# Optimization experiments

Hardware: AMD Instinct MI355X
Metric: run time of the kernel (lower is better)

Reference implementation:

```python
import jax, jax.numpy as jnp
import numpy as np

B = 16          # graphs per batch
NN = 2000       # nodes per graph (num_nodes)
N = B * NN      # total nodes in the batched graph
F_IN = 128      # input node features
H, C = 4, 64    # heads, per-head out channels (both GAT layers)
HC = H * C
DEG = 12        # average degree per node
FC1, FC2, OUT = 512, 128, 1
FC_IN = 6 * NN  # len(which_layer) = 6


def setup_inputs() -> dict:
    key = jax.random.key(0)
    ks = jax.random.split(key, 32)

    def g(i, shape, s=0.05):
        return jax.random.normal(ks[i], shape, jnp.float32) * s

    # within-graph random edges, no self loops (GATConv removes then re-adds them)
    src_l = jax.random.randint(ks[0], (B, NN * DEG), 0, NN)
    off = jax.random.randint(ks[1], (B, NN * DEG), 1, NN)
    dst_l = (src_l + off) % NN
    goff = (jnp.arange(B) * NN)[:, None]
    edge_index = jnp.stack([(src_l + goff).reshape(-1),
                            (dst_l + goff).reshape(-1)]).astype(jnp.int32)

    return {
        "x": g(2, (N, F_IN), 1.0),
        "W1": g(3, (F_IN, HC)), "att_src1": g(4, (H, C)), "att_dst1": g(5, (H, C)),
        "b1": jnp.zeros((HC,), jnp.float32),
        "W2": g(6, (HC, HC)), "att_src2": g(7, (H, C)), "att_dst2": g(8, (H, C)),
        "b2": jnp.zeros((HC,), jnp.float32),
        "pw1": g(9, (HC, 1)), "pb1": jnp.zeros((1,), jnp.float32),
        "pw2": g(10, (HC, 1)), "pb2": jnp.zeros((1,), jnp.float32),
        "ln_w": jnp.ones((NN,), jnp.float32), "ln_b": jnp.zeros((NN,), jnp.float32),
        "sex_emb": g(11, (2, NN)), "mut_emb": g(12, (4, NN)),
        "age_w": g(13, (NN,)), "age_b": jnp.zeros((NN,), jnp.float32),
        "fw1": g(14, (FC_IN, FC1)), "fb1": jnp.zeros((FC1,), jnp.float32),
        "fw2": g(15, (FC1, FC2)), "fb2": jnp.zeros((FC2,), jnp.float32),
        "fw3": g(16, (FC2, OUT)), "fb3": jnp.zeros((OUT,), jnp.float32),
        "age": jax.random.uniform(ks[17], (B,), jnp.float32),
        "edge_index": edge_index,
        "sex": jax.random.randint(ks[18], (B,), 0, 2),
        "mutation": jax.random.randint(ks[19], (B,), 0, 4),
    }


def _layer_norm(x, w, b, eps=1e-5):
    mu = jnp.mean(x, -1, keepdims=True)
    var = jnp.mean((x - mu) ** 2, -1, keepdims=True)
    return (x - mu) / jnp.sqrt(var + eps) * w + b


def _gat_conv(x, W, att_src, att_dst, bias, src, dst):
    h = (x @ W).reshape(N, H, C)                         # [N,H,C]
    a_s = jnp.sum(h * att_src[None], -1)                 # [N,H]
    a_d = jnp.sum(h * att_dst[None], -1)                 # [N,H]
    alpha = jax.nn.leaky_relu(a_s[src] + a_d[dst], 0.2)  # [E,H]
    m = jax.ops.segment_max(alpha, dst, num_segments=N)  # segment softmax over dst
    e = jnp.exp(alpha - m[dst])
    denom = jax.ops.segment_sum(e, dst, num_segments=N)
    a = e / (denom[dst] + 1e-16)
    out = jax.ops.segment_sum(a[:, :, None] * h[src], dst, num_segments=N)
    return out.reshape(N, HC) + bias


def _forward(x, W1, att_src1, att_dst1, b1, W2, att_src2, att_dst2, b2,
             pw1, pb1, pw2, pb2, ln_w, ln_b, sex_emb, mut_emb, age_w, age_b,
             fw1, fb1, fw2, fb2, fw3, fb3, age, edge_index, sex, mutation):
    loop = jnp.arange(N, dtype=edge_index.dtype)         # self loops added by GATConv
    src = jnp.concatenate([edge_index[0], loop])
    dst = jnp.concatenate([edge_index[1], loop])

    x0 = jnp.mean(x, -1).reshape(B, NN)                  # to_dense_batch(mean(x,-1))

    h = jax.nn.relu(_gat_conv(x, W1, att_src1, att_dst1, b1, src, dst))
    x1 = (h @ pw1 + pb1).squeeze(-1).reshape(B, NN)
    h = jax.nn.relu(_gat_conv(h, W2, att_src2, att_dst2, b2, src, dst))
    x2 = (h @ pw2 + pb2).squeeze(-1).reshape(B, NN)

    x0 = _layer_norm(x0, ln_w, ln_b)
    x1 = _layer_norm(x1, ln_w, ln_b)
    x2 = _layer_norm(x2, ln_w, ln_b)
    ms = jnp.concatenate([x0, x1, x2], axis=1)           # [B, 3*NN]

    demo = jnp.concatenate([sex_emb[sex], mut_emb[mutation],
                            age[:, None] * age_w[None, :] + age_b], axis=1)
    t = jnp.concatenate([demo, ms], axis=1)              # [B, 6*NN]
    t = jax.nn.relu(t @ fw1 + fb1)
    t = jax.nn.relu(t @ fw2 + fb2)
    pred = t @ fw3 + fb3                                 # [B, 1]
    return pred, x0, x1, x2, ms


def reference(x, W1, att_src1, att_dst1, b1, W2, att_src2, att_dst2, b2,
              pw1, pb1, pw2, pb2, ln_w, ln_b, sex_emb, mut_emb, age_w, age_b,
              fw1, fb1, fw2, fb2, fw3, fb3, age, edge_index, sex, mutation):
    return _forward(x, W1, att_src1, att_dst1, b1, W2, att_src2, att_dst2, b2,
                    pw1, pb1, pw2, pb2, ln_w, ln_b, sex_emb, mut_emb, age_w, age_b,
                    fw1, fb1, fw2, fb2, fw3, fb3, age, edge_index, sex, mutation)
```

## Files before the change

kernel.cpp:

```cpp
#include <hip/hip_runtime.h>
#include <math.h>

#define NTOT   32000
#define NNODE  2000
#define NB     16
#define FIN    128
#define HCDIM  256
#define NH     4
#define FC1DIM 512
#define FC2DIM 128
#define FCIN   12000
#define NCH    250
#define KCC    48
#define CAP    64
#define BK     32
#define LPITCH 40
#define TRB2   24
#define DEMOB  375

typedef __attribute__((ext_vector_type(8))) short bf16x8;
typedef __attribute__((ext_vector_type(4))) float f32x4;

__device__ inline float4 ld4(const float* p){ return *reinterpret_cast<const float4*>(p); }
__device__ inline void st4(float* p, float4 v){ *reinterpret_cast<float4*>(p) = v; }
__device__ inline float4 add4(float4 a, float4 b){ return make_float4(a.x+b.x,a.y+b.y,a.z+b.z,a.w+b.w); }
__device__ inline float lrelu(float x){ return x > 0.f ? x : 0.2f*x; }
__device__ inline float4 leaky4(float4 a){ return make_float4(lrelu(a.x),lrelu(a.y),lrelu(a.z),lrelu(a.w)); }
__device__ inline float4 exp4u(float4 a){ return make_float4(__expf(a.x),__expf(a.y),__expf(a.z),__expf(a.w)); }
__device__ inline float dot4(float4 a, float4 b){ return a.x*b.x + a.y*b.y + a.z*b.z + a.w*b.w; }
__device__ inline float selh(float4 v, int h){ return h==0 ? v.x : (h==1 ? v.y : (h==2 ? v.z : v.w)); }

__device__ inline unsigned short f2bf(float f){
  unsigned int u = __float_as_uint(f);
  u += 0x7FFFu + ((u >> 16) & 1u);
  return (unsigned short)(u >> 16);
}
__device__ inline unsigned int pk2bf(float a, float b){
  return (unsigned int)f2bf(a) | ((unsigned int)f2bf(b) << 16);
}
__device__ inline float bf2f(unsigned short h){
  return __uint_as_float(((unsigned int)h) << 16);
}
__device__ inline float4 ldbf4(const unsigned short* p){
  ushort4 v = *reinterpret_cast<const ushort4*>(p);
  return make_float4(bf2f(v.x), bf2f(v.y), bf2f(v.z), bf2f(v.w));
}

__global__ __launch_bounds__(256) void k_zero(int* __restrict__ cnt){
  int i = blockIdx.x*256 + threadIdx.x;
  if(i < NTOT) cnt[i] = 0;
}

__device__ __forceinline__ void ln_impl(const float* __restrict__ src,
                                        const float* __restrict__ lnw,
                                        const float* __restrict__ lnb,
                                        float* __restrict__ o1,
                                        float* __restrict__ o2,
                                        float* __restrict__ o3,
                                        float* red){
  int tid = threadIdx.x, lane = tid & 63, wv = tid >> 6;
  float s = 0.f, ss = 0.f;
  for(int i = tid; i < NNODE; i += 256){ float v = src[i]; s += v; ss += v*v; }
  #pragma unroll
  for(int off=1; off<64; off<<=1){ s += __shfl_xor(s, off); ss += __shfl_xor(ss, off); }
  if(lane == 0){ red[wv] = s; red[4+wv] = ss; }
  __syncthreads();
  s  = red[0]+red[1]+red[2]+red[3];
  ss = red[4]+red[5]+red[6]+red[7];
  float mu  = s * (1.0f/NNODE);
  float var = ss * (1.0f/NNODE) - mu*mu;
  float inv = 1.0f / sqrtf(var + 1e-5f);
  for(int i = tid; i < NNODE; i += 256){
    float v = (src[i]-mu)*inv*lnw[i] + lnb[i];
    o1[i] = v; o2[i] = v; o3[i] = v;
  }
}

__global__ void k_misc(const int* __restrict__ src, const int* __restrict__ dst,
                       int* __restrict__ cnt, int* __restrict__ col, int e0, int eb,
                       const float* __restrict__ W1, const float* __restrict__ W2,
                       unsigned short* __restrict__ W1t, unsigned short* __restrict__ W2t,
                       const float* __restrict__ sexemb, const float* __restrict__ mutemb,
                       const float* __restrict__ agew, const float* __restrict__ ageb,
                       const float* __restrict__ age, const int* __restrict__ sex,
                       const int* __restrict__ mut, float* __restrict__ t){
  __shared__ float tile[64][65];
  int blk = blockIdx.x;
  if(blk < eb){
    int i = blk*256 + threadIdx.x;
    if(i < e0){
      int d = dst[i];
      int slot = atomicAdd(&cnt[d], 1);
      if(slot < CAP) col[(d<<6) + slot] = src[i];
    }
  } else if(blk < eb + TRB2){
    int tb = blk - eb;
    int wv = threadIdx.x >> 6, lane = threadIdx.x & 63;
    if(tb < 8){
      int tk = tb >> 2, tn = tb & 3;
      int k0 = tk*64, n0 = tn*64;
      #pragma unroll
      for(int q=0;q<16;q++){
        int row = q*4 + wv;
        tile[row][lane] = W1[(size_t)(k0+row)*HCDIM + n0 + lane];
      }
      __syncthreads();
      #pragma unroll
      for(int q=0;q<16;q++){
        int row = q*4 + wv;
        W1t[(size_t)(n0+row)*FIN + k0 + lane] = f2bf(tile[lane][row]);
      }
    } else {
      int t2 = tb - 8;
      int tk = t2 >> 2, tn = t2 & 3;
      int k0 = tk*64, n0 = tn*64;
      #pragma unroll
      for(int q=0;q<16;q++){
        int row = q*4 + wv;
        tile[row][lane] = W2[(size_t)(k0+row)*HCDIM + n0 + lane];
      }
      __syncthreads();
      #pragma unroll
      for(int q=0;q<16;q++){
        int row = q*4 + wv;
        W2t[(size_t)(n0+row)*HCDIM + k0 + lane] = f2bf(tile[lane][row]);
      }
    }
  } else {
    int i = (blk - eb - TRB2)*256 + threadIdx.x;
    int b = i / (3*NNODE);
    int j = i - b*(3*NNODE);
    float v;
    if(j < NNODE)          v = sexemb[sex[b]*NNODE + j];
    else if(j < 2*NNODE)   v = mutemb[mut[b]*NNODE + (j - NNODE)];
    else                   v = age[b]*agew[j - 2*NNODE] + ageb[j - 2*NNODE];
    t[b*FCIN + j] = v;
  }
}

template<int AF32>
__global__ __launch_bounds__(256) void k_gemm_bf(const void* __restrict__ Av,
                                                 const unsigned short* __restrict__ Bt,
                                                 unsigned short* __restrict__ C,
                                                 const float* __restrict__ attS,
                                                 const float* __restrict__ attD,
                                                 float* __restrict__ a_s,
                                                 float* __restrict__ a_d,
                                                 float* __restrict__ x0r,
                                                 int M, int K){
  const unsigned short* A = (const unsigned short*)Av;
  const float*         Af = (const float*)Av;
  __shared__ unsigned short As[128][LPITCH];
  __shared__ unsigned short Bs[128][LPITCH];
  int tid = threadIdx.x;
  int lane = tid & 63, wv = tid >> 6;
  int wm = (wv & 1)*64, wn = (wv >> 1)*64;
  int m0 = blockIdx.y*128, n0 = blockIdx.x*128;
  int l15 = lane & 15, lq = lane >> 4;
  f32x4 acc[4][4];
  #pragma unroll
  for(int i=0;i<4;i++)
    #pragma unroll
    for(int j=0;j<4;j++)
      acc[i][j] = (f32x4){0.f,0.f,0.f,0.f};

  int r = tid >> 2, c = (tid & 3)*8;
  float rs1 = 0.f, rs2 = 0.f;
  for(int k0 = 0; k0 < K; k0 += BK){
    if(AF32){
      const float* pa  = Af + (size_t)(m0+r)*K + k0 + c;
      const float* pa2 = Af + (size_t)(m0+r+64)*K + k0 + c;
      float4 u0 = ld4(pa),  u1 = ld4(pa+4);
      float4 v0 = ld4(pa2), v1 = ld4(pa2+4);
      rs1 += (u0.x+u0.y+u0.z+u0.w) + (u1.x+u1.y+u1.z+u1.w);
      rs2 += (v0.x+v0.y+v0.z+v0.w) + (v1.x+v1.y+v1.z+v1.w);
      uint4 w0, w1;
      w0.x = pk2bf(u0.x,u0.y); w0.y = pk2bf(u0.z,u0.w);
      w0.z = pk2bf(u1.x,u1.y); w0.w = pk2bf(u1.z,u1.w);
      w1.x = pk2bf(v0.x,v0.y); w1.y = pk2bf(v0.z,v0.w);
      w1.z = pk2bf(v1.x,v1.y); w1.w = pk2bf(v1.z,v1.w);
      *reinterpret_cast<uint4*>(&As[r][c])    = w0;
      *reinterpret_cast<uint4*>(&As[r+64][c]) = w1;
    } else {
      *reinterpret_cast<uint4*>(&As[r][c])    = *reinterpret_cast<const uint4*>(A  + (size_t)(m0+r)*K + k0 + c);
      *reinterpret_cast<uint4*>(&As[r+64][c]) = *reinterpret_cast<const uint4*>(A  + (size_t)(m0+r+64)*K + k0 + c);
    }
    *reinterpret_cast<uint4*>(&Bs[r][c])    = *reinterpret_cast<const uint4*>(Bt + (size_t)(n0+r)*K + k0 + c);
    *reinterpret_cast<uint4*>(&Bs[r+64][c]) = *reinterpret_cast<const uint4*>(Bt + (size_t)(n0+r+64)*K + k0 + c);
    __syncthreads();
    bf16x8 af[4], bfr[4];
    #pragma unroll
    for(int i=0;i<4;i++){
      af[i]  = *reinterpret_cast<const bf16x8*>(&As[wm + i*16 + l15][lq*8]);
      bfr[i] = *reinterpret_cast<const bf16x8*>(&Bs[wn + i*16 + l15][lq*8]);
    }
    #pragma unroll
    for(int mi=0;mi<4;mi++)
      #pragma unroll
      for(int ni=0;ni<4;ni++)
        acc[mi][ni] = __builtin_amdgcn_mfma_f32_16x16x32_bf16(af[mi], bfr[ni], acc[mi][ni], 0, 0, 0);
    __syncthreads();
  }
  if(AF32 && n0 == 0){
    float s1 = rs1, s2 = rs2;
    s1 += __shfl_xor(s1,1); s1 += __shfl_xor(s1,2);
    s2 += __shfl_xor(s2,1); s2 += __shfl_xor(s2,2);
    if((tid & 3) == 0){
      x0r[m0 + r]      = s1 * (1.0f/FIN);
      x0r[m0 + r + 64] = s2 * (1.0f/FIN);
    }
  }
  #pragma unroll
  for(int mi=0;mi<4;mi++){
    #pragma unroll
    for(int ni=0;ni<4;ni++){
      int cn = n0 + wn + ni*16 + l15;
      #pragma unroll
      for(int rg=0;rg<4;rg++){
        int rm = m0 + wm + mi*16 + lq*4 + rg;
        C[(size_t)rm*HCDIM + cn] = f2bf(acc[mi][ni][rg]);
      }
    }
  }
  int head = (n0 + wn) >> 6;
  float avs[4], avd[4];
  #pragma unroll
  for(int ni=0;ni<4;ni++){
    int cc = ni*16 + l15;
    avs[ni] = attS[head*64 + cc];
    avd[ni] = attD[head*64 + cc];
  }
  #pragma unroll
  for(int mi=0;mi<4;mi++){
    #pragma unroll
    for(int rg=0;rg<4;rg++){
      float ps = 0.f, pd = 0.f;
      #pragma unroll
      for(int ni=0;ni<4;ni++){
        float v = acc[mi][ni][rg];
        ps = fmaf(avs[ni], v, ps);
        pd = fmaf(avd[ni], v, pd);
      }
      #pragma unroll
      for(int off=1; off<16; off<<=1){
        ps += __shfl_xor(ps, off);
        pd += __shfl_xor(pd, off);
      }
      if(l15 == 0){
        int rm = m0 + wm + mi*16 + lq*4 + rg;
        a_s[rm*4 + head] = ps;
        a_d[rm*4 + head] = pd;
      }
    }
  }
}

template<int STORE>
__global__ __launch_bounds__(256) void k_agg(const unsigned short* __restrict__ hpre,
                                             const float* __restrict__ a_s,
                                             const float* __restrict__ a_d,
                                             const int* __restrict__ cnt,
                                             const int* __restrict__ col,
                                             const float* __restrict__ bias,
                                             const float* __restrict__ pw,
                                             const float* __restrict__ pb,
                                             unsigned short* __restrict__ hout,
                                             float* __restrict__ xraw,
                                             const float* __restrict__ lnsrc,
                                             const float* __restrict__ lnw,
                                             const float* __restrict__ lnb,
                                             float* __restrict__ out,
                                             float* __restrict__ t,
                                             int which){
  __shared__ float4 ew[4][CAP];
  __shared__ int    cols[4][CAP+1];
  __shared__ float  lred[8];
  int bx = blockIdx.x;
  if(bx < 16){
    int b = bx;
    ln_impl(lnsrc + b*NNODE, lnw, lnb,
            out + 16 + which*(NB*NNODE) + b*NNODE,
            out + 16 + 3*(NB*NNODE) + b*(3*NNODE) + which*NNODE,
            t + b*FCIN + 3*NNODE + which*NNODE, lred);
    return;
  }
  int tid = threadIdx.x;
  int lane = tid & 63, wv = tid >> 6;
  int blk  = bx - 16;
  int xcd  = blk & 7;
  int slot = blk >> 3;
  int half = slot / 500;
  int g    = xcd + 8*half;
  int n    = g*NNODE + (slot - half*500)*4 + wv;
  int f0 = lane*4;
  int hl = lane >> 4;
  float4 ad   = ld4(a_d + n*4);
  float4 asn  = ld4(a_s + n*4);
  float4 eself = exp4u(leaky4(add4(asn, ad)));
  int deg = min(cnt[n], CAP);
  int base = n << 6;
  if(lane < deg){
    int s = col[base + lane];
    cols[wv][lane] = s;
    ew[wv][lane] = exp4u(leaky4(add4(ld4(a_s + s*4), ad)));
  } else {
    cols[wv][lane] = n;
  }
  if(lane == 0) cols[wv][CAP] = n;
  float es = selh(eself, hl);
  float dsum = es;
  float4 hv = ldbf4(hpre + (size_t)n*HCDIM + f0);
  float4 acc = make_float4(es*hv.x, es*hv.y, es*hv.z, es*hv.w);
  const float* ewf = (const float*)&ew[wv][0];
  const int*   cwf = &cols[wv][0];
  float4 h2 = ldbf4(hpre + (size_t)cwf[0]*HCDIM + f0);
  for(int e = 0; e < deg; e++){
    int sn = cwf[e+1];
    float4 hn = ldbf4(hpre + (size_t)sn*HCDIM + f0);
    float w = ewf[e*4 + hl];
    dsum += w;
    acc.x = fmaf(w, h2.x, acc.x); acc.y = fmaf(w, h2.y, acc.y);
    acc.z = fmaf(w, h2.z, acc.z); acc.w = fmaf(w, h2.w, acc.w);
    h2 = hn;
  }
  float invh = 1.0f / (dsum + 1e-16f);
  float4 b4 = ld4(bias + f0);
  acc = make_float4(fmaxf(fmaf(acc.x,invh,b4.x),0.f), fmaxf(fmaf(acc.y,invh,b4.y),0.f),
                    fmaxf(fmaf(acc.z,invh,b4.z),0.f), fmaxf(fmaf(acc.w,invh,b4.w),0.f));
  if(STORE){
    ushort4 hb = make_ushort4(f2bf(acc.x), f2bf(acc.y), f2bf(acc.z), f2bf(acc.w));
    *reinterpret_cast<ushort4*>(hout + (size_t)n*HCDIM + f0) = hb;
  }
  float part = dot4(acc, ld4(pw + f0));
  #pragma unroll
  for(int off=1; off<64; off<<=1) part += __shfl_xor(part, off);
  if(lane == 0) xraw[n] = part + pb[0];
}

__global__ __launch_bounds__(256) void k_lnx2(const float* __restrict__ x2r,
                                              const float* __restrict__ lnw,
                                              const float* __restrict__ lnb,
                                              float* __restrict__ out,
                                              float* __restrict__ t){
  __shared__ float red[8];
  int b = blockIdx.x;
  ln_impl(x2r + b*NNODE, lnw, lnb,
          out + 16 + 2*(NB*NNODE) + b*NNODE,
          out + 16 + 3*(NB*NNODE) + b*(3*NNODE) + 2*NNODE,
          t + b*FCIN + 3*NNODE + 2*NNODE, red);
}

__global__ __launch_bounds__(256) void k_fc1(const float* __restrict__ t,
                                             const float* __restrict__ fw1,
                                             float* __restrict__ partial){
  __shared__ float ts[NB][KCC];
  int blk = blockIdx.x;
  int chunk = blk >> 1;
  int halfc = blk & 1;
  int tid = threadIdx.x;
  int k0 = chunk * KCC;
  for(int i = tid; i < NB*KCC; i += 256){
    int b = i / KCC, kk = i - b*KCC;
    ts[b][kk] = t[b*FCIN + k0 + kk];
  }
  __syncthreads();
  int j = halfc*256 + tid;
  float acc[NB];
  #pragma unroll
  for(int b=0;b<NB;b++) acc[b] = 0.f;
  const float* wp = fw1 + (size_t)k0*FC1DIM + j;
  #pragma unroll 8
  for(int kk = 0; kk < KCC; kk++){
    float w = wp[(size_t)kk*FC1DIM];
    #pragma unroll
    for(int b=0;b<NB;b++) acc[b] = fmaf(ts[b][kk], w, acc[b]);
  }
  float* po = partial + (size_t)chunk*(NB*FC1DIM) + j;
  #pragma unroll
  for(int b=0;b<NB;b++) po[b*FC1DIM] = acc[b];
}

__global__ __launch_bounds__(256) void k_fc1r(const float* __restrict__ partial,
                                              const float* __restrict__ fb1,
                                              float* __restrict__ t1){
  __shared__ float red[3][64];
  int tid = threadIdx.x;
  int e = blockIdx.x*64 + (tid & 63);
  int g = tid >> 6;
  int c0 = (g < 2) ? g*63 : 126 + (g-2)*62;
  int cn = (g < 2) ? 63 : 62;
  float s = 0.f;
  for(int c = c0; c < c0 + cn; c++) s += partial[(size_t)c*(NB*FC1DIM) + e];
  if(g) red[g-1][tid & 63] = s;
  __syncthreads();
  if(g == 0){
    s += red[0][tid & 63] + red[1][tid & 63] + red[2][tid & 63];
    s += fb1[e & (FC1DIM-1)];
    t1[e] = fmaxf(s, 0.f);
  }
}

__global__ __launch_bounds__(128) void k_head2(const float* __restrict__ t1,
                                               const float* __restrict__ fw2,
                                               const float* __restrict__ fb2,
                                               const float* __restrict__ fw3,
                                               const float* __restrict__ fb3,
                                               float* __restrict__ pred){
  __shared__ float red[2];
  int b = blockIdx.x, j = threadIdx.x;
  const float* tr = t1 + b*FC1DIM;
  float s = fb2[j];
  for(int k=0;k<FC1DIM;k++) s = fmaf(tr[k], fw2[k*FC2DIM+j], s);
  s = fmaxf(s, 0.f) * fw3[j];
  #pragma unroll
  for(int off=1; off<64; off<<=1) s += __shfl_xor(s, off);
  int lane = j & 63, wv = j >> 6;
  if(lane == 0) red[wv] = s;
  __syncthreads();
  if(j == 0) pred[b] = red[0] + red[1] + fb3[0];
}

extern "C" void kernel_launch(void* const* d_in, const int* in_sizes, int n_in,
                              void* d_out, int out_size, void* d_ws, size_t ws_size,
                              hipStream_t stream) {
  const float* x       = (const float*)d_in[0];
  const float* W1      = (const float*)d_in[1];
  const float* attS1   = (const float*)d_in[2];
  const float* attD1   = (const float*)d_in[3];
  const float* b1      = (const float*)d_in[4];
  const float* W2      = (const float*)d_in[5];
  const float* attS2   = (const float*)d_in[6];
  const float* attD2   = (const float*)d_in[7];
  const float* b2      = (const float*)d_in[8];
  const float* pw1     = (const float*)d_in[9];
  const float* pb1     = (const float*)d_in[10];
  const float* pw2     = (const float*)d_in[11];
  const float* pb2     = (const float*)d_in[12];
  const float* lnw     = (const float*)d_in[13];
  const float* lnb     = (const float*)d_in[14];
  const float* sexemb  = (const float*)d_in[15];
  const float* mutemb  = (const float*)d_in[16];
  const float* agew    = (const float*)d_in[17];
  const float* ageb    = (const float*)d_in[18];
  const float* fw1     = (const float*)d_in[19];
  const float* fb1     = (const float*)d_in[20];
  const float* fw2     = (const float*)d_in[21];
  const float* fb2     = (const float*)d_in[22];
  const float* fw3     = (const float*)d_in[23];
  const float* fb3     = (const float*)d_in[24];
  const float* age     = (const float*)d_in[25];
  const int*   eidx    = (const int*)d_in[26];
  const int*   sex     = (const int*)d_in[27];
  const int*   mut     = (const int*)d_in[28];
  const int E0 = in_sizes[26] / 2;
  const int* esrc = eidx;
  const int* edst = eidx + E0;

  float* out = (float*)d_out;

  float* w = (float*)d_ws;
  float* a_s  = w;
  float* a_d  = a_s + NTOT*NH;
  float* x0r  = a_d + NTOT*NH;
  float* x1r  = x0r + NTOT;
  float* x2r  = x1r + NTOT;
  float* tbuf = x2r + NTOT;
  float* part = tbuf + NB*FCIN;
  float* t1   = part + (size_t)256*NB*FC1DIM;
  unsigned short* hA  = (unsigned short*)(t1 + NB*FC1DIM);
  unsigned short* hB  = hA  + (size_t)NTOT*HCDIM;
  unsigned short* W1t = hB  + (size_t)NTOT*HCDIM;
  unsigned short* W2t = W1t + HCDIM*FIN;
  int* cnt    = (int*)(W2t + HCDIM*HCDIM);
  int* col    = cnt + NTOT;
  (void)ws_size; (void)n_in; (void)out_size;

  const int eb = (E0 + 255)/256;

  k_zero<<<(NTOT+255)/256, 256, 0, stream>>>(cnt);
  k_misc<<<eb + TRB2 + DEMOB, 256, 0, stream>>>(esrc, edst, cnt, col, E0, eb,
                                               W1, W2, W1t, W2t,
                                               sexemb, mutemb, agew, ageb,
                                               age, sex, mut, tbuf);

  k_gemm_bf<1><<<dim3(HCDIM/128, NTOT/128), 256, 0, stream>>>(x, W1t, hA, attS1, attD1, a_s, a_d, x0r, NTOT, FIN);
  k_agg<1><<<16 + NTOT/4, 256, 0, stream>>>(hA, a_s, a_d, cnt, col, b1, pw1, pb1, hB, x1r,
                                            x0r, lnw, lnb, out, tbuf, 0);

  k_gemm_bf<0><<<dim3(HCDIM/128, NTOT/128), 256, 0, stream>>>(hB, W2t, hA, attS2, attD2, a_s, a_d, (float*)0, NTOT, HCDIM);
  k_agg<0><<<16 + NTOT/4, 256, 0, stream>>>(hA, a_s, a_d, cnt, col, b2, pw2, pb2, hB, x2r,
                                            x1r, lnw, lnb, out, tbuf, 1);

  k_lnx2<<<NB, 256, 0, stream>>>(x2r, lnw, lnb, out, tbuf);

  k_fc1<<<NCH*2, 256, 0, stream>>>(tbuf, fw1, part);
  k_fc1r<<<(NB*FC1DIM)/64, 256, 0, stream>>>(part, fb1, t1);
  k_head2<<<NB, 128, 0, stream>>>(t1, fw2, fb2, fw3, fb3, out);
}
```

Before: 279.3 us.

## Fuse all stages into one persistent kernel with software grid barriers

Replaces the chain of separate launches (zero, misc, two GEMMs, two aggregations, LN, FC1, reduction, head) with one persistent kernel of 512 blocks. The stages are separated by atomic-counter grid barriers. Edge bucketing now runs in the same phase as the first GEMM, after the counters are zeroed. This is meant to remove launch gaps and tail effects between the many small kernels. In exchange it relies on all 512 blocks being co-resident, loops blocks over roles, and adds a spin barrier with a timeout guard that could silently break correctness if residency fails.

```diff
diff --git a/kernel.cpp b/kernel.cpp
--- a/kernel.cpp
+++ b/kernel.cpp
@@ -17,12 +17,14 @@
 #define LPITCH 40
 #define TRB2   24
 #define DEMOB  375
+#define ZB     125
+#define NBLK   512
+#define SPIN_MAX 20000000
 
 typedef __attribute__((ext_vector_type(8))) short bf16x8;
 typedef __attribute__((ext_vector_type(4))) float f32x4;
 
 __device__ inline float4 ld4(const float* p){ return *reinterpret_cast<const float4*>(p); }
-__device__ inline void st4(float* p, float4 v){ *reinterpret_cast<float4*>(p) = v; }
 __device__ inline float4 add4(float4 a, float4 b){ return make_float4(a.x+b.x,a.y+b.y,a.z+b.z,a.w+b.w); }
 __device__ inline float lrelu(float x){ return x > 0.f ? x : 0.2f*x; }
 __device__ inline float4 leaky4(float4 a){ return make_float4(lrelu(a.x),lrelu(a.y),lrelu(a.z),lrelu(a.w)); }
@@ -46,9 +48,34 @@
   return make_float4(bf2f(v.x), bf2f(v.y), bf2f(v.z), bf2f(v.w));
 }
 
-__global__ __launch_bounds__(256) void k_zero(int* __restrict__ cnt){
-  int i = blockIdx.x*256 + threadIdx.x;
-  if(i < NTOT) cnt[i] = 0;
+struct MegaParams {
+  const float *x, *W1, *attS1, *attD1, *b1;
+  const float *W2, *attS2, *attD2, *b2;
+  const float *pw1, *pb1, *pw2, *pb2;
+  const float *lnw, *lnb, *sexemb, *mutemb, *agew, *ageb;
+  const float *fw1, *fb1, *fw2, *fb2, *fw3, *fb3, *age;
+  const int *esrc, *edst, *sex, *mut;
+  float *out;
+  float *a_s, *a_d, *x0r, *x1r, *x2r, *tbuf, *part, *t1;
+  unsigned short *hA, *hB, *W1t, *W2t;
+  int *cnt, *col;
+  unsigned int *bar;
+  int E0, eb;
+};
+
+__device__ __forceinline__ void gridbar(unsigned int* bar){
+  __syncthreads();
+  if(threadIdx.x == 0){
+    __threadfence();
+    unsigned int old = __hip_atomic_fetch_add(bar, 1u, __ATOMIC_ACQ_REL, __HIP_MEMORY_SCOPE_AGENT);
+    unsigned int target = (old/NBLK + 1u) * (unsigned int)NBLK;
+    int guard = 0;
+    while(__hip_atomic_load(bar, __ATOMIC_ACQUIRE, __HIP_MEMORY_SCOPE_AGENT) < target){
+      if(++guard > SPIN_MAX) break;
+    }
+    __threadfence();
+  }
+  __syncthreads();
 }
 
 __device__ __forceinline__ void ln_impl(const float* __restrict__ src,
@@ -74,88 +101,22 @@
     float v = (src[i]-mu)*inv*lnw[i] + lnb[i];
     o1[i] = v; o2[i] = v; o3[i] = v;
   }
-}
-
-__global__ void k_misc(const int* __restrict__ src, const int* __restrict__ dst,
-                       int* __restrict__ cnt, int* __restrict__ col, int e0, int eb,
-                       const float* __restrict__ W1, const float* __restrict__ W2,
-                       unsigned short* __restrict__ W1t, unsigned short* __restrict__ W2t,
-                       const float* __restrict__ sexemb, const float* __restrict__ mutemb,
-                       const float* __restrict__ agew, const float* __restrict__ ageb,
-                       const float* __restrict__ age, const int* __restrict__ sex,
-                       const int* __restrict__ mut, float* __restrict__ t){
-  __shared__ float tile[64][65];
-  int blk = blockIdx.x;
-  if(blk < eb){
-    int i = blk*256 + threadIdx.x;
-    if(i < e0){
-      int d = dst[i];
-      int slot = atomicAdd(&cnt[d], 1);
-      if(slot < CAP) col[(d<<6) + slot] = src[i];
-    }
-  } else if(blk < eb + TRB2){
-    int tb = blk - eb;
-    int wv = threadIdx.x >> 6, lane = threadIdx.x & 63;
-    if(tb < 8){
-      int tk = tb >> 2, tn = tb & 3;
-      int k0 = tk*64, n0 = tn*64;
-      #pragma unroll
-      for(int q=0;q<16;q++){
-        int row = q*4 + wv;
-        tile[row][lane] = W1[(size_t)(k0+row)*HCDIM + n0 + lane];
-      }
-      __syncthreads();
-      #pragma unroll
-      for(int q=0;q<16;q++){
-        int row = q*4 + wv;
-        W1t[(size_t)(n0+row)*FIN + k0 + lane] = f2bf(tile[lane][row]);
-      }
-    } else {
-      int t2 = tb - 8;
-      int tk = t2 >> 2, tn = t2 & 3;
-      int k0 = tk*64, n0 = tn*64;
-      #pragma unroll
-      for(int q=0;q<16;q++){
-        int row = q*4 + wv;
-        tile[row][lane] = W2[(size_t)(k0+row)*HCDIM + n0 + lane];
-      }
-      __syncthreads();
-      #pragma unroll
-      for(int q=0;q<16;q++){
-        int row = q*4 + wv;
-        W2t[(size_t)(n0+row)*HCDIM + k0 + lane] = f2bf(tile[lane][row]);
-      }
-    }
-  } else {
-    int i = (blk - eb - TRB2)*256 + threadIdx.x;
-    int b = i / (3*NNODE);
-    int j = i - b*(3*NNODE);
-    float v;
-    if(j < NNODE)          v = sexemb[sex[b]*NNODE + j];
-    else if(j < 2*NNODE)   v = mutemb[mut[b]*NNODE + (j - NNODE)];
-    else                   v = age[b]*agew[j - 2*NNODE] + ageb[j - 2*NNODE];
-    t[b*FCIN + j] = v;
-  }
+  __syncthreads();
 }
 
 template<int AF32>
-__global__ __launch_bounds__(256) void k_gemm_bf(const void* __restrict__ Av,
-                                                 const unsigned short* __restrict__ Bt,
-                                                 unsigned short* __restrict__ C,
-                                                 const float* __restrict__ attS,
-                                                 const float* __restrict__ attD,
-                                                 float* __restrict__ a_s,
-                                                 float* __restrict__ a_d,
-                                                 float* __restrict__ x0r,
-                                                 int M, int K){
+__device__ __forceinline__ void gemm_tile(const MegaParams& p, int rl, char* smraw,
+                                          const void* Av, const unsigned short* Bt,
+                                          unsigned short* C, const float* attS,
+                                          const float* attD, int K){
   const unsigned short* A = (const unsigned short*)Av;
   const float*         Af = (const float*)Av;
-  __shared__ unsigned short As[128][LPITCH];
-  __shared__ unsigned short Bs[128][LPITCH];
+  unsigned short (*As)[LPITCH] = (unsigned short(*)[LPITCH])smraw;
+  unsigned short (*Bs)[LPITCH] = (unsigned short(*)[LPITCH])(smraw + 128*LPITCH*2);
   int tid = threadIdx.x;
   int lane = tid & 63, wv = tid >> 6;
   int wm = (wv & 1)*64, wn = (wv >> 1)*64;
-  int m0 = blockIdx.y*128, n0 = blockIdx.x*128;
+  int n0 = (rl & 1)*128, m0 = (rl >> 1)*128;
   int l15 = lane & 15, lq = lane >> 4;
   f32x4 acc[4][4];
   #pragma unroll
@@ -206,8 +167,8 @@
     s1 += __shfl_xor(s1,1); s1 += __shfl_xor(s1,2);
     s2 += __shfl_xor(s2,1); s2 += __shfl_xor(s2,2);
     if((tid & 3) == 0){
-      x0r[m0 + r]      = s1 * (1.0f/FIN);
-      x0r[m0 + r + 64] = s2 * (1.0f/FIN);
+      p.x0r[m0 + r]      = s1 * (1.0f/FIN);
+      p.x0r[m0 + r + 64] = s2 * (1.0f/FIN);
     }
   }
   #pragma unroll
@@ -248,43 +209,31 @@
       }
       if(l15 == 0){
         int rm = m0 + wm + mi*16 + lq*4 + rg;
-        a_s[rm*4 + head] = ps;
-        a_d[rm*4 + head] = pd;
+        p.a_s[rm*4 + head] = ps;
+        p.a_d[rm*4 + head] = pd;
       }
     }
   }
 }
 
 template<int STORE>
-__global__ __launch_bounds__(256) void k_agg(const unsigned short* __restrict__ hpre,
-                                             const float* __restrict__ a_s,
-                                             const float* __restrict__ a_d,
-                                             const int* __restrict__ cnt,
-                                             const int* __restrict__ col,
-                                             const float* __restrict__ bias,
-                                             const float* __restrict__ pw,
-                                             const float* __restrict__ pb,
-                                             unsigned short* __restrict__ hout,
-                                             float* __restrict__ xraw,
-                                             const float* __restrict__ lnsrc,
-                                             const float* __restrict__ lnw,
-                                             const float* __restrict__ lnb,
-                                             float* __restrict__ out,
-                                             float* __restrict__ t,
-                                             int which){
-  __shared__ float4 ew[4][CAP];
-  __shared__ int    cols[4][CAP+1];
-  __shared__ float  lred[8];
-  int bx = blockIdx.x;
+__device__ __forceinline__ void agg_role(const MegaParams& p, int bx, char* smraw,
+                                         const unsigned short* hpre, const float* bias,
+                                         const float* pw, const float* pb,
+                                         unsigned short* hout, float* xraw,
+                                         const float* lnsrc, int which){
+  float4 (*ew)[CAP]    = (float4(*)[CAP])smraw;
+  int    (*cols)[CAP+1]= (int(*)[CAP+1])(smraw + 4096);
+  float*  lred         = (float*)(smraw + 5152);
+  int tid = threadIdx.x;
   if(bx < 16){
     int b = bx;
-    ln_impl(lnsrc + b*NNODE, lnw, lnb,
-            out + 16 + which*(NB*NNODE) + b*NNODE,
-            out + 16 + 3*(NB*NNODE) + b*(3*NNODE) + which*NNODE,
-            t + b*FCIN + 3*NNODE + which*NNODE, lred);
+    ln_impl(lnsrc + b*NNODE, p.lnw, p.lnb,
+            p.out + 16 + which*(NB*NNODE) + b*NNODE,
+            p.out + 16 + 3*(NB*NNODE) + b*(3*NNODE) + which*NNODE,
+            p.tbuf + b*FCIN + 3*NNODE + which*NNODE, lred);
     return;
   }
-  int tid = threadIdx.x;
   int lane = tid & 63, wv = tid >> 6;
   int blk  = bx - 16;
   int xcd  = blk & 7;
@@ -294,15 +243,15 @@
   int n    = g*NNODE + (slot - half*500)*4 + wv;
   int f0 = lane*4;
   int hl = lane >> 4;
-  float4 ad   = ld4(a_d + n*4);
-  float4 asn  = ld4(a_s + n*4);
+  float4 ad   = ld4(p.a_d + n*4);
+  float4 asn  = ld4(p.a_s + n*4);
   float4 eself = exp4u(leaky4(add4(asn, ad)));
-  int deg = min(cnt[n], CAP);
+  int deg = min(p.cnt[n], CAP);
   int base = n << 6;
   if(lane < deg){
-    int s = col[base + lane];
+    int s = p.col[base + lane];
     cols[wv][lane] = s;
-    ew[wv][lane] = exp4u(leaky4(add4(ld4(a_s + s*4), ad)));
+    ew[wv][lane] = exp4u(leaky4(add4(ld4(p.a_s + s*4), ad)));
   } else {
     cols[wv][lane] = n;
   }
@@ -337,163 +286,228 @@
   if(lane == 0) xraw[n] = part + pb[0];
 }
 
-__global__ __launch_bounds__(256) void k_lnx2(const float* __restrict__ x2r,
-                                              const float* __restrict__ lnw,
-                                              const float* __restrict__ lnb,
-                                              float* __restrict__ out,
-                                              float* __restrict__ t){
-  __shared__ float red[8];
-  int b = blockIdx.x;
-  ln_impl(x2r + b*NNODE, lnw, lnb,
-          out + 16 + 2*(NB*NNODE) + b*NNODE,
-          out + 16 + 3*(NB*NNODE) + b*(3*NNODE) + 2*NNODE,
-          t + b*FCIN + 3*NNODE + 2*NNODE, red);
-}
-
-__global__ __launch_bounds__(256) void k_fc1(const float* __restrict__ t,
-                                             const float* __restrict__ fw1,
-                                             float* __restrict__ partial){
-  __shared__ float ts[NB][KCC];
-  int blk = blockIdx.x;
-  int chunk = blk >> 1;
-  int halfc = blk & 1;
-  int tid = threadIdx.x;
-  int k0 = chunk * KCC;
-  for(int i = tid; i < NB*KCC; i += 256){
-    int b = i / KCC, kk = i - b*KCC;
-    ts[b][kk] = t[b*FCIN + k0 + kk];
-  }
-  __syncthreads();
-  int j = halfc*256 + tid;
-  float acc[NB];
-  #pragma unroll
-  for(int b=0;b<NB;b++) acc[b] = 0.f;
-  const float* wp = fw1 + (size_t)k0*FC1DIM + j;
-  #pragma unroll 8
-  for(int kk = 0; kk < KCC; kk++){
-    float w = wp[(size_t)kk*FC1DIM];
-    #pragma unroll
-    for(int b=0;b<NB;b++) acc[b] = fmaf(ts[b][kk], w, acc[b]);
-  }
-  float* po = partial + (size_t)chunk*(NB*FC1DIM) + j;
-  #pragma unroll
-  for(int b=0;b<NB;b++) po[b*FC1DIM] = acc[b];
-}
-
-__global__ __launch_bounds__(256) void k_fc1r(const float* __restrict__ partial,
-                                              const float* __restrict__ fb1,
-                                              float* __restrict__ t1){
-  __shared__ float red[3][64];
-  int tid = threadIdx.x;
-  int e = blockIdx.x*64 + (tid & 63);
-  int g = tid >> 6;
-  int c0 = (g < 2) ? g*63 : 126 + (g-2)*62;
-  int cn = (g < 2) ? 63 : 62;
-  float s = 0.f;
-  for(int c = c0; c < c0 + cn; c++) s += partial[(size_t)c*(NB*FC1DIM) + e];
-  if(g) red[g-1][tid & 63] = s;
-  __syncthreads();
-  if(g == 0){
-    s += red[0][tid & 63] + red[1][tid & 63] + red[2][tid & 63];
-    s += fb1[e & (FC1DIM-1)];
-    t1[e] = fmaxf(s, 0.f);
-  }
-}
-
-__global__ __launch_bounds__(128) void k_head2(const float* __restrict__ t1,
-                                               const float* __restrict__ fw2,
-                                               const float* __restrict__ fb2,
-                                               const float* __restrict__ fw3,
-                                               const float* __restrict__ fb3,
-                                               float* __restrict__ pred){
-  __shared__ float red[2];
-  int b = blockIdx.x, j = threadIdx.x;
-  const float* tr = t1 + b*FC1DIM;
-  float s = fb2[j];
-  for(int k=0;k<FC1DIM;k++) s = fmaf(tr[k], fw2[k*FC2DIM+j], s);
-  s = fmaxf(s, 0.f) * fw3[j];
-  #pragma unroll
-  for(int off=1; off<64; off<<=1) s += __shfl_xor(s, off);
-  int lane = j & 63, wv = j >> 6;
-  if(lane == 0) red[wv] = s;
-  __syncthreads();
-  if(j == 0) pred[b] = red[0] + red[1] + fb3[0];
+__global__ void k_init(unsigned int* bar){ if(threadIdx.x == 0) *bar = 0u; }
+
+__global__ __launch_bounds__(256, 2) void k_mega(MegaParams p){
+  __shared__ __align__(16) char smraw[20608];
+  const int tid = threadIdx.x;
+  const int bid = blockIdx.x;
+  const int lane = tid & 63, wvi = tid >> 6;
+
+  for(int role = bid; role < ZB + TRB2 + DEMOB; role += NBLK){
+    if(role < ZB){
+      int i = role*256 + tid;
+      if(i < NTOT) p.cnt[i] = 0;
+    } else if(role < ZB + TRB2){
+      float (*tile)[65] = (float(*)[65])smraw;
+      int tb = role - ZB;
+      if(tb < 8){
+        int tk = tb >> 2, tn = tb & 3;
+        int k0 = tk*64, n0 = tn*64;
+        #pragma unroll
+        for(int q=0;q<16;q++){
+          int row = q*4 + wvi;
+          tile[row][lane] = p.W1[(size_t)(k0+row)*HCDIM + n0 + lane];
+        }
+        __syncthreads();
+        #pragma unroll
+        for(int q=0;q<16;q++){
+          int row = q*4 + wvi;
+          p.W1t[(size_t)(n0+row)*FIN + k0 + lane] = f2bf(tile[lane][row]);
+        }
+        __syncthreads();
+      } else {
+        int t2 = tb - 8;
+        int tk = t2 >> 2, tn = t2 & 3;
+        int k0 = tk*64, n0 = tn*64;
+        #pragma unroll
+        for(int q=0;q<16;q++){
+          int row = q*4 + wvi;
+          tile[row][lane] = p.W2[(size_t)(k0+row)*HCDIM + n0 + lane];
+        }
+        __syncthreads();
+        #pragma unroll
+        for(int q=0;q<16;q++){
+          int row = q*4 + wvi;
+          p.W2t[(size_t)(n0+row)*HCDIM + k0 + lane] = f2bf(tile[lane][row]);
+        }
+        __syncthreads();
+      }
+    } else {
+      int i = (role - ZB - TRB2)*256 + tid;
+      int b = i / (3*NNODE);
+      int j = i - b*(3*NNODE);
+      float v;
+      if(j < NNODE)          v = p.sexemb[p.sex[b]*NNODE + j];
+      else if(j < 2*NNODE)   v = p.mutemb[p.mut[b]*NNODE + (j - NNODE)];
+      else                   v = p.age[b]*p.agew[j - 2*NNODE] + p.ageb[j - 2*NNODE];
+      p.tbuf[b*FCIN + j] = v;
+    }
+  }
+  gridbar(p.bar);
+
+  {
+    int R1 = p.eb + 500;
+    for(int role = bid; role < R1; role += NBLK){
+      if(role < p.eb){
+        int i = role*256 + tid;
+        if(i < p.E0){
+          int d = p.edst[i];
+          int slot = atomicAdd(&p.cnt[d], 1);
+          if(slot < CAP) p.col[(d<<6) + slot] = p.esrc[i];
+        }
+      } else {
+        gemm_tile<1>(p, role - p.eb, smraw, p.x, p.W1t, p.hA, p.attS1, p.attD1, FIN);
+      }
+    }
+  }
+  gridbar(p.bar);
+
+  for(int role = bid; role < 16 + NTOT/4; role += NBLK)
+    agg_role<1>(p, role, smraw, p.hA, p.b1, p.pw1, p.pb1, p.hB, p.x1r, p.x0r, 0);
+  gridbar(p.bar);
+
+  for(int role = bid; role < 500; role += NBLK)
+    gemm_tile<0>(p, role, smraw, p.hB, p.W2t, p.hA, p.attS2, p.attD2, HCDIM);
+  gridbar(p.bar);
+
+  for(int role = bid; role < 16 + NTOT/4; role += NBLK)
+    agg_role<0>(p, role, smraw, p.hA, p.b2, p.pw2, p.pb2, p.hB, p.x2r, p.x1r, 1);
+  gridbar(p.bar);
+
+  for(int role = bid; role < 16; role += NBLK){
+    float* red = (float*)smraw;
+    ln_impl(p.x2r + role*NNODE, p.lnw, p.lnb,
+            p.out + 16 + 2*(NB*NNODE) + role*NNODE,
+            p.out + 16 + 3*(NB*NNODE) + role*(3*NNODE) + 2*NNODE,
+            p.tbuf + role*FCIN + 3*NNODE + 2*NNODE, red);
+  }
+  gridbar(p.bar);
+
+  for(int role = bid; role < 2*NCH; role += NBLK){
+    float (*ts)[KCC] = (float(*)[KCC])smraw;
+    int chunk = role >> 1;
+    int halfc = role & 1;
+    int k0 = chunk * KCC;
+    for(int i = tid; i < NB*KCC; i += 256){
+      int b = i / KCC, kk = i - b*KCC;
+      ts[b][kk] = p.tbuf[b*FCIN + k0 + kk];
+    }
+    __syncthreads();
+    int j = halfc*256 + tid;
+    float acc[NB];
+    #pragma unroll
+    for(int b=0;b<NB;b++) acc[b] = 0.f;
+    const float* wp = p.fw1 + (size_t)k0*FC1DIM + j;
+    #pragma unroll 8
+    for(int kk = 0; kk < KCC; kk++){
+      float w = wp[(size_t)kk*FC1DIM];
+      #pragma unroll
+      for(int b=0;b<NB;b++) acc[b] = fmaf(ts[b][kk], w, acc[b]);
+    }
+    float* po = p.part + (size_t)chunk*(NB*FC1DIM) + j;
+    #pragma unroll
+    for(int b=0;b<NB;b++) po[b*FC1DIM] = acc[b];
+    __syncthreads();
+  }
+  gridbar(p.bar);
+
+  for(int role = bid; role < (NB*FC1DIM)/64; role += NBLK){
+    float (*red)[64] = (float(*)[64])smraw;
+    int e = role*64 + (tid & 63);
+    int g = tid >> 6;
+    int c0 = (g < 2) ? g*63 : 126 + (g-2)*62;
+    int cn = (g < 2) ? 63 : 62;
+    float s = 0.f;
+    for(int c = c0; c < c0 + cn; c++) s += p.part[(size_t)c*(NB*FC1DIM) + e];
+    if(g) red[g-1][tid & 63] = s;
+    __syncthreads();
+    if(g == 0){
+      s += red[0][tid & 63] + red[1][tid & 63] + red[2][tid & 63];
+      s += p.fb1[e & (FC1DIM-1)];
+      p.t1[e] = fmaxf(s, 0.f);
+    }
+    __syncthreads();
+  }
+  gridbar(p.bar);
+
+  for(int role = bid; role < NB; role += NBLK){
+    float* red2 = (float*)smraw;
+    int b = role;
+    float s = 0.f;
+    if(tid < FC2DIM){
+      int j = tid;
+      const float* tr = p.t1 + b*FC1DIM;
+      s = p.fb2[j];
+      for(int k=0;k<FC1DIM;k++) s = fmaf(tr[k], p.fw2[k*FC2DIM+j], s);
+      s = fmaxf(s, 0.f) * p.fw3[j];
+      #pragma unroll
+      for(int off=1; off<64; off<<=1) s += __shfl_xor(s, off);
+      if((tid & 63) == 0) red2[tid >> 6] = s;
+    }
+    __syncthreads();
+    if(tid == 0) p.out[b] = red2[0] + red2[1] + p.fb3[0];
+    __syncthreads();
+  }
 }
 
 extern "C" void kernel_launch(void* const* d_in, const int* in_sizes, int n_in,
                               void* d_out, int out_size, void* d_ws, size_t ws_size,
                               hipStream_t stream) {
-  const float* x       = (const float*)d_in[0];
-  const float* W1      = (const float*)d_in[1];
-  const float* attS1   = (const float*)d_in[2];
-  const float* attD1   = (const float*)d_in[3];
-  const float* b1      = (const float*)d_in[4];
-  const float* W2      = (const float*)d_in[5];
-  const float* attS2   = (const float*)d_in[6];
-  const float* attD2   = (const float*)d_in[7];
-  const float* b2      = (const float*)d_in[8];
-  const float* pw1     = (const float*)d_in[9];
-  const float* pb1     = (const float*)d_in[10];
-  const float* pw2     = (const float*)d_in[11];
-  const float* pb2     = (const float*)d_in[12];
-  const float* lnw     = (const float*)d_in[13];
-  const float* lnb     = (const float*)d_in[14];
-  const float* sexemb  = (const float*)d_in[15];
-  const float* mutemb  = (const float*)d_in[16];
-  const float* agew    = (const float*)d_in[17];
-  const float* ageb    = (const float*)d_in[18];
-  const float* fw1     = (const float*)d_in[19];
-  const float* fb1     = (const float*)d_in[20];
-  const float* fw2     = (const float*)d_in[21];
-  const float* fb2     = (const float*)d_in[22];
-  const float* fw3     = (const float*)d_in[23];
-  const float* fb3     = (const float*)d_in[24];
-  const float* age     = (const float*)d_in[25];
-  const int*   eidx    = (const int*)d_in[26];
-  const int*   sex     = (const int*)d_in[27];
-  const int*   mut     = (const int*)d_in[28];
-  const int E0 = in_sizes[26] / 2;
-  const int* esrc = eidx;
-  const int* edst = eidx + E0;
-
-  float* out = (float*)d_out;
+  MegaParams p;
+  p.x      = (const float*)d_in[0];
+  p.W1     = (const float*)d_in[1];
+  p.attS1  = (const float*)d_in[2];
+  p.attD1  = (const float*)d_in[3];
+  p.b1     = (const float*)d_in[4];
+  p.W2     = (const float*)d_in[5];
+  p.attS2  = (const float*)d_in[6];
+  p.attD2  = (const float*)d_in[7];
+  p.b2     = (const float*)d_in[8];
+  p.pw1    = (const float*)d_in[9];
+  p.pb1    = (const float*)d_in[10];
+  p.pw2    = (const float*)d_in[11];
+  p.pb2    = (const float*)d_in[12];
+  p.lnw    = (const float*)d_in[13];
+  p.lnb    = (const float*)d_in[14];
+  p.sexemb = (const float*)d_in[15];
+  p.mutemb = (const float*)d_in[16];
+  p.agew   = (const float*)d_in[17];
+  p.ageb   = (const float*)d_in[18];
+  p.fw1    = (const float*)d_in[19];
+  p.fb1    = (const float*)d_in[20];
+  p.fw2    = (const float*)d_in[21];
+  p.fb2    = (const float*)d_in[22];
+  p.fw3    = (const float*)d_in[23];
+  p.fb3    = (const float*)d_in[24];
+  p.age    = (const float*)d_in[25];
+  const int* eidx = (const int*)d_in[26];
+  p.sex    = (const int*)d_in[27];
+  p.mut    = (const int*)d_in[28];
+  p.E0   = in_sizes[26] / 2;
+  p.esrc = eidx;
+  p.edst = eidx + p.E0;
+  p.eb   = (p.E0 + 255)/256;
+  p.out  = (float*)d_out;
 
   float* w = (float*)d_ws;
-  float* a_s  = w;
-  float* a_d  = a_s + NTOT*NH;
-  float* x0r  = a_d + NTOT*NH;
-  float* x1r  = x0r + NTOT;
-  float* x2r  = x1r + NTOT;
-  float* tbuf = x2r + NTOT;
-  float* part = tbuf + NB*FCIN;
-  float* t1   = part + (size_t)256*NB*FC1DIM;
-  unsigned short* hA  = (unsigned short*)(t1 + NB*FC1DIM);
-  unsigned short* hB  = hA  + (size_t)NTOT*HCDIM;
-  unsigned short* W1t = hB  + (size_t)NTOT*HCDIM;
-  unsigned short* W2t = W1t + HCDIM*FIN;
-  int* cnt    = (int*)(W2t + HCDIM*HCDIM);
-  int* col    = cnt + NTOT;
+  p.a_s  = w;
+  p.a_d  = p.a_s + NTOT*NH;
+  p.x0r  = p.a_d + NTOT*NH;
+  p.x1r  = p.x0r + NTOT;
+  p.x2r  = p.x1r + NTOT;
+  p.tbuf = p.x2r + NTOT;
+  p.part = p.tbuf + NB*FCIN;
+  p.t1   = p.part + (size_t)256*NB*FC1DIM;
+  p.hA   = (unsigned short*)(p.t1 + NB*FC1DIM);
+  p.hB   = p.hA + (size_t)NTOT*HCDIM;
+  p.W1t  = p.hB + (size_t)NTOT*HCDIM;
+  p.W2t  = p.W1t + HCDIM*FIN;
+  p.cnt  = (int*)(p.W2t + HCDIM*HCDIM);
+  p.col  = p.cnt + NTOT;
+  p.bar  = (unsigned int*)(p.col + (size_t)NTOT*CAP);
   (void)ws_size; (void)n_in; (void)out_size;
 
-  const int eb = (E0 + 255)/256;
-
-  k_zero<<<(NTOT+255)/256, 256, 0, stream>>>(cnt);
-  k_misc<<<eb + TRB2 + DEMOB, 256, 0, stream>>>(esrc, edst, cnt, col, E0, eb,
-                                               W1, W2, W1t, W2t,
-                                               sexemb, mutemb, agew, ageb,
-                                               age, sex, mut, tbuf);
-
-  k_gemm_bf<1><<<dim3(HCDIM/128, NTOT/128), 256, 0, stream>>>(x, W1t, hA, attS1, attD1, a_s, a_d, x0r, NTOT, FIN);
-  k_agg<1><<<16 + NTOT/4, 256, 0, stream>>>(hA, a_s, a_d, cnt, col, b1, pw1, pb1, hB, x1r,
-                                            x0r, lnw, lnb, out, tbuf, 0);
-
-  k_gemm_bf<0><<<dim3(HCDIM/128, NTOT/128), 256, 0, stream>>>(hB, W2t, hA, attS2, attD2, a_s, a_d, (float*)0, NTOT, HCDIM);
-  k_agg<0><<<16 + NTOT/4, 256, 0, stream>>>(hA, a_s, a_d, cnt, col, b2, pw2, pb2, hB, x2r,
-                                            x1r, lnw, lnb, out, tbuf, 1);
-
-  k_lnx2<<<NB, 256, 0, stream>>>(x2r, lnw, lnb, out, tbuf);
-
-  k_fc1<<<NCH*2, 256, 0, stream>>>(tbuf, fw1, part);
-  k_fc1r<<<(NB*FC1DIM)/64, 256, 0, stream>>>(part, fb1, t1);
-  k_head2<<<NB, 128, 0, stream>>>(t1, fw2, fb2, fw3, fb3, out);
-}
+  k_init<<<1, 64, 0, stream>>>(p.bar);
+  k_mega<<<NBLK, 256, 0, stream>>>(p);
+}
```

Result: slower. 1.013 ms (+262.6%).

## Merge small kernels into role-split launches to cut launch count

Applied to the files above, without the earlier changes.

Folds counter zeroing into the prep kernel, moves the edge-to-CSR scatter into the first GEMM launch as extra blocks, and combines the x2 layer norm with the fc1 chunks that do not depend on x2. The fc1 chunks that read the x2 columns run in a separate follow-up launch. The goal is to remove launch gaps and let independent work share the GPU, at the cost of more intricate block-role dispatch and hard-coded split points.

```diff
diff --git a/kernel.cpp b/kernel.cpp
--- a/kernel.cpp
+++ b/kernel.cpp
@@ -15,14 +15,16 @@
 #define CAP    64
 #define BK     32
 #define LPITCH 40
+#define ZB     125
 #define TRB2   24
 #define DEMOB  375
+#define FC1A   416
+#define FC1B   84
 
 typedef __attribute__((ext_vector_type(8))) short bf16x8;
 typedef __attribute__((ext_vector_type(4))) float f32x4;
 
 __device__ inline float4 ld4(const float* p){ return *reinterpret_cast<const float4*>(p); }
-__device__ inline void st4(float* p, float4 v){ *reinterpret_cast<float4*>(p) = v; }
 __device__ inline float4 add4(float4 a, float4 b){ return make_float4(a.x+b.x,a.y+b.y,a.z+b.z,a.w+b.w); }
 __device__ inline float lrelu(float x){ return x > 0.f ? x : 0.2f*x; }
 __device__ inline float4 leaky4(float4 a){ return make_float4(lrelu(a.x),lrelu(a.y),lrelu(a.z),lrelu(a.w)); }
@@ -44,11 +46,6 @@
 __device__ inline float4 ldbf4(const unsigned short* p){
   ushort4 v = *reinterpret_cast<const ushort4*>(p);
   return make_float4(bf2f(v.x), bf2f(v.y), bf2f(v.z), bf2f(v.w));
-}
-
-__global__ __launch_bounds__(256) void k_zero(int* __restrict__ cnt){
-  int i = blockIdx.x*256 + threadIdx.x;
-  if(i < NTOT) cnt[i] = 0;
 }
 
 __device__ __forceinline__ void ln_impl(const float* __restrict__ src,
@@ -76,8 +73,7 @@
   }
 }
 
-__global__ void k_misc(const int* __restrict__ src, const int* __restrict__ dst,
-                       int* __restrict__ cnt, int* __restrict__ col, int e0, int eb,
+__global__ __launch_bounds__(256) void k_prep(int* __restrict__ cnt,
                        const float* __restrict__ W1, const float* __restrict__ W2,
                        unsigned short* __restrict__ W1t, unsigned short* __restrict__ W2t,
                        const float* __restrict__ sexemb, const float* __restrict__ mutemb,
@@ -86,15 +82,10 @@
                        const int* __restrict__ mut, float* __restrict__ t){
   __shared__ float tile[64][65];
   int blk = blockIdx.x;
-  if(blk < eb){
-    int i = blk*256 + threadIdx.x;
-    if(i < e0){
-      int d = dst[i];
-      int slot = atomicAdd(&cnt[d], 1);
-      if(slot < CAP) col[(d<<6) + slot] = src[i];
-    }
-  } else if(blk < eb + TRB2){
-    int tb = blk - eb;
+  if(blk < ZB){
+    cnt[blk*256 + threadIdx.x] = 0;
+  } else if(blk < ZB + TRB2){
+    int tb = blk - ZB;
     int wv = threadIdx.x >> 6, lane = threadIdx.x & 63;
     if(tb < 8){
       int tk = tb >> 2, tn = tb & 3;
@@ -127,7 +118,7 @@
       }
     }
   } else {
-    int i = (blk - eb - TRB2)*256 + threadIdx.x;
+    int i = (blk - ZB - TRB2)*256 + threadIdx.x;
     int b = i / (3*NNODE);
     int j = i - b*(3*NNODE);
     float v;
@@ -139,23 +130,19 @@
 }
 
 template<int AF32>
-__global__ __launch_bounds__(256) void k_gemm_bf(const void* __restrict__ Av,
-                                                 const unsigned short* __restrict__ Bt,
-                                                 unsigned short* __restrict__ C,
-                                                 const float* __restrict__ attS,
-                                                 const float* __restrict__ attD,
-                                                 float* __restrict__ a_s,
-                                                 float* __restrict__ a_d,
-                                                 float* __restrict__ x0r,
-                                                 int M, int K){
+__device__ __forceinline__ void gemm_tile(int rl, char* smraw,
+                                          const void* Av, const unsigned short* Bt,
+                                          unsigned short* C, const float* attS,
+                                          const float* attD, float* a_s, float* a_d,
+                                          float* x0r, int K){
   const unsigned short* A = (const unsigned short*)Av;
   const float*         Af = (const float*)Av;
-  __shared__ unsigned short As[128][LPITCH];
-  __shared__ unsigned short Bs[128][LPITCH];
+  unsigned short (*As)[LPITCH] = (unsigned short(*)[LPITCH])smraw;
+  unsigned short (*Bs)[LPITCH] = (unsigned short(*)[LPITCH])(smraw + 128*LPITCH*2);
   int tid = threadIdx.x;
   int lane = tid & 63, wv = tid >> 6;
   int wm = (wv & 1)*64, wn = (wv >> 1)*64;
-  int m0 = blockIdx.y*128, n0 = blockIdx.x*128;
+  int n0 = (rl & 1)*128, m0 = (rl >> 1)*128;
   int l15 = lane & 15, lq = lane >> 4;
   f32x4 acc[4][4];
   #pragma unroll
@@ -253,6 +240,43 @@
       }
     }
   }
+}
+
+__global__ __launch_bounds__(256) void k_bg1(const float* __restrict__ x,
+                                             const unsigned short* __restrict__ W1t,
+                                             unsigned short* __restrict__ hA,
+                                             const float* __restrict__ attS1,
+                                             const float* __restrict__ attD1,
+                                             float* __restrict__ a_s,
+                                             float* __restrict__ a_d,
+                                             float* __restrict__ x0r,
+                                             const int* __restrict__ esrc,
+                                             const int* __restrict__ edst,
+                                             int* __restrict__ cnt,
+                                             int* __restrict__ col, int E0){
+  __shared__ __align__(16) char smraw[128*LPITCH*4];
+  int bid = blockIdx.x;
+  if(bid < 500){
+    gemm_tile<1>(bid, smraw, x, W1t, hA, attS1, attD1, a_s, a_d, x0r, FIN);
+  } else {
+    int i = (bid - 500)*256 + threadIdx.x;
+    if(i < E0){
+      int d = edst[i];
+      int slot = atomicAdd(&cnt[d], 1);
+      if(slot < CAP) col[(d<<6) + slot] = esrc[i];
+    }
+  }
+}
+
+__global__ __launch_bounds__(256) void k_gemm2(const unsigned short* __restrict__ hB,
+                                               const unsigned short* __restrict__ W2t,
+                                               unsigned short* __restrict__ hA,
+                                               const float* __restrict__ attS2,
+                                               const float* __restrict__ attD2,
+                                               float* __restrict__ a_s,
+                                               float* __restrict__ a_d){
+  __shared__ __align__(16) char smraw[128*LPITCH*4];
+  gemm_tile<0>(blockIdx.x, smraw, hB, W2t, hA, attS2, attD2, a_s, a_d, (float*)0, HCDIM);
 }
 
 template<int STORE>
@@ -337,26 +361,13 @@
   if(lane == 0) xraw[n] = part + pb[0];
 }
 
-__global__ __launch_bounds__(256) void k_lnx2(const float* __restrict__ x2r,
-                                              const float* __restrict__ lnw,
-                                              const float* __restrict__ lnb,
-                                              float* __restrict__ out,
-                                              float* __restrict__ t){
-  __shared__ float red[8];
-  int b = blockIdx.x;
-  ln_impl(x2r + b*NNODE, lnw, lnb,
-          out + 16 + 2*(NB*NNODE) + b*NNODE,
-          out + 16 + 3*(NB*NNODE) + b*(3*NNODE) + 2*NNODE,
-          t + b*FCIN + 3*NNODE + 2*NNODE, red);
-}
-
-__global__ __launch_bounds__(256) void k_fc1(const float* __restrict__ t,
-                                             const float* __restrict__ fw1,
-                                             float* __restrict__ partial){
-  __shared__ float ts[NB][KCC];
-  int blk = blockIdx.x;
-  int chunk = blk >> 1;
-  int halfc = blk & 1;
+__device__ __forceinline__ void fc1_role(int role, float* tsraw,
+                                         const float* __restrict__ t,
+                                         const float* __restrict__ fw1,
+                                         float* __restrict__ partial){
+  float (*ts)[KCC] = (float(*)[KCC])tsraw;
+  int chunk = role >> 1;
+  int halfc = role & 1;
   int tid = threadIdx.x;
   int k0 = chunk * KCC;
   for(int i = tid; i < NB*KCC; i += 256){
@@ -378,6 +389,34 @@
   float* po = partial + (size_t)chunk*(NB*FC1DIM) + j;
   #pragma unroll
   for(int b=0;b<NB;b++) po[b*FC1DIM] = acc[b];
+}
+
+__global__ __launch_bounds__(256) void k_tailA(const float* __restrict__ x2r,
+                                               const float* __restrict__ lnw,
+                                               const float* __restrict__ lnb,
+                                               float* __restrict__ out,
+                                               float* __restrict__ t,
+                                               const float* __restrict__ fw1,
+                                               float* __restrict__ partial){
+  __shared__ __align__(16) float tsraw[NB*KCC];
+  __shared__ float red[8];
+  int bx = blockIdx.x;
+  if(bx < 16){
+    int b = bx;
+    ln_impl(x2r + b*NNODE, lnw, lnb,
+            out + 16 + 2*(NB*NNODE) + b*NNODE,
+            out + 16 + 3*(NB*NNODE) + b*(3*NNODE) + 2*NNODE,
+            t + b*FCIN + 3*NNODE + 2*NNODE, red);
+    return;
+  }
+  fc1_role(bx - 16, tsraw, t, fw1, partial);
+}
+
+__global__ __launch_bounds__(256) void k_fc1b(const float* __restrict__ t,
+                                              const float* __restrict__ fw1,
+                                              float* __restrict__ partial){
+  __shared__ __align__(16) float tsraw[NB*KCC];
+  fc1_role(FC1A + blockIdx.x, tsraw, t, fw1, partial);
 }
 
 __global__ __launch_bounds__(256) void k_fc1r(const float* __restrict__ partial,
@@ -477,23 +516,26 @@
 
   const int eb = (E0 + 255)/256;
 
-  k_zero<<<(NTOT+255)/256, 256, 0, stream>>>(cnt);
-  k_misc<<<eb + TRB2 + DEMOB, 256, 0, stream>>>(esrc, edst, cnt, col, E0, eb,
-                                               W1, W2, W1t, W2t,
-                                               sexemb, mutemb, agew, ageb,
-                                               age, sex, mut, tbuf);
-
-  k_gemm_bf<1><<<dim3(HCDIM/128, NTOT/128), 256, 0, stream>>>(x, W1t, hA, attS1, attD1, a_s, a_d, x0r, NTOT, FIN);
+  k_prep<<<ZB + TRB2 + DEMOB, 256, 0, stream>>>(cnt, W1, W2, W1t, W2t,
+                                                sexemb, mutemb, agew, ageb,
+                                                age, sex, mut, tbuf);
+
+  k_bg1<<<500 + eb, 256, 0, stream>>>(x, W1t, hA, attS1, attD1, a_s, a_d, x0r,
+                                      esrc, edst, cnt, col, E0);
+
   k_agg<1><<<16 + NTOT/4, 256, 0, stream>>>(hA, a_s, a_d, cnt, col, b1, pw1, pb1, hB, x1r,
                                             x0r, lnw, lnb, out, tbuf, 0);
 
-  k_gemm_bf<0><<<dim3(HCDIM/128, NTOT/128), 256, 0, stream>>>(hB, W2t, hA, attS2, attD2, a_s, a_d, (float*)0, NTOT, HCDIM);
+  k_gemm2<<<500, 256, 0, stream>>>(hB, W2t, hA, attS2, attD2, a_s, a_d);
+
   k_agg<0><<<16 + NTOT/4, 256, 0, stream>>>(hA, a_s, a_d, cnt, col, b2, pw2, pb2, hB, x2r,
                                             x1r, lnw, lnb, out, tbuf, 1);
 
-  k_lnx2<<<NB, 256, 0, stream>>>(x2r, lnw, lnb, out, tbuf);
-
-  k_fc1<<<NCH*2, 256, 0, stream>>>(tbuf, fw1, part);
+  k_tailA<<<16 + FC1A, 256, 0, stream>>>(x2r, lnw, lnb, out, tbuf, fw1, part);
+
+  k_fc1b<<<FC1B, 256, 0, stream>>>(tbuf, fw1, part);
+
   k_fc1r<<<(NB*FC1DIM)/64, 256, 0, stream>>>(part, fb1, t1);
+
   k_head2<<<NB, 128, 0, stream>>>(t1, fw2, fb2, fw3, fb3, out);
 }
```

New measurement: 285.8 us. 2.3% more time.
